# Performance work log

Measured on AMD Instinct MI355X. Metric: run time of the kernel, lower is better.

Reference implementation:

```python
import jax, jax.numpy as jnp
import numpy as np

# Dimensions (match init_kwargs / input_specs)
N, C_IN, C, H, W = 2, 256, 256, 80, 80
G, KS = 16, 3                 # groups, kernel_size
K = KS * KS                   # sampling points per group
CG = C // G                   # channels per group
PAD, STRIDE, DIL = 1, 1, 1
OFFSET_SCALE = 1.0
EPS = 1e-5                    # BatchNorm2d eps (eval mode)


def setup_inputs() -> dict:
    key = jax.random.key(0)
    ks = jax.random.split(key, 12)
    rn = lambda k, shape, s=0.02: jax.random.normal(k, shape, dtype=jnp.float32) * s
    return {
        "x": jax.random.normal(ks[0], (N, C_IN, H, W), dtype=jnp.float32),
        # Conv(inc, ouc, k=1): 1x1 conv (bias=False) + BN + SiLU
        "w1": rn(ks[1], (C_IN, C)),
        "bn1_g": jnp.ones((C,), jnp.float32), "bn1_b": jnp.zeros((C,), jnp.float32),
        "bn1_m": rn(ks[2], (C,), 0.1),
        "bn1_v": jax.random.uniform(ks[3], (C,), minval=0.5, maxval=1.5, dtype=jnp.float32),
        # DCNv4: value_proj, fused offset_mask, output_proj
        "wv": rn(ks[4], (C, C)), "bv": jnp.zeros((C,), jnp.float32),
        "wom": rn(ks[5], (C, G * K * 3)), "bom": rn(ks[6], (G * K * 3,), 0.1),
        "wo": rn(ks[7], (C, C)), "bo": jnp.zeros((C,), jnp.float32),
        # trailing BatchNorm2d + SiLU
        "bn2_g": jnp.ones((C,), jnp.float32), "bn2_b": jnp.zeros((C,), jnp.float32),
        "bn2_m": rn(ks[8], (C,), 0.1),
        "bn2_v": jax.random.uniform(ks[9], (C,), minval=0.5, maxval=1.5, dtype=jnp.float32),
    }


def _bn(x, g, b, m, v):
    # eval-mode BatchNorm over last (channel) axis
    return (x - m) * jax.lax.rsqrt(v + EPS) * g + b


def _forward(x, w1, bn1_g, bn1_b, bn1_m, bn1_v, wv, bv, wom, bom, wo, bo,
             bn2_g, bn2_b, bn2_m, bn2_v):
    # --- Conv 1x1 + BN + SiLU (channels-last) ---
    h = jnp.einsum('nchw,cd->nhwd', x, w1)                 # (N,H,W,C)
    h = jax.nn.silu(_bn(h, bn1_g, bn1_b, bn1_m, bn1_v))

    # --- DCNv4 ---
    xf = h.reshape(N, H * W, C)
    value = (xf @ wv + bv).reshape(N, H, W, G, CG)         # value projection
    om = (xf @ wom + bom).reshape(N, H, W, G, 3 * K)       # fused offset+mask
    offset = om[..., :2 * K].reshape(N, H, W, G, K, 2) * OFFSET_SCALE  # (x,y) pairs
    mask = om[..., 2 * K:]                                 # (N,H,W,G,K); v4: no softmax

    # sampling pixel coords: p = out_pos*stride - pad + kernel_offset*dil + learned offset
    ky, kx = jnp.meshgrid(jnp.arange(KS), jnp.arange(KS), indexing='ij')
    ky = (ky.reshape(-1) * DIL).astype(jnp.float32)        # (K,)
    kx = (kx.reshape(-1) * DIL).astype(jnp.float32)
    base_y = (jnp.arange(H) * STRIDE - PAD).astype(jnp.float32)
    base_x = (jnp.arange(W) * STRIDE - PAD).astype(jnp.float32)
    py = base_y[None, :, None, None, None] + ky[None, None, None, None, :] + offset[..., 1]
    px = base_x[None, None, :, None, None] + kx[None, None, None, None, :] + offset[..., 0]

    y0 = jnp.floor(py); x0 = jnp.floor(px)
    wy = py - y0;       wx = px - x0
    y0i = y0.astype(jnp.int32); x0i = x0.astype(jnp.int32)
    y1i = y0i + 1;             x1i = x0i + 1

    ni = jnp.arange(N)[:, None, None, None, None]
    gi = jnp.arange(G)[None, None, None, :, None]

    def gather(yi, xi):
        valid = ((yi >= 0) & (yi < H) & (xi >= 0) & (xi < W)).astype(value.dtype)
        v = value[ni, jnp.clip(yi, 0, H - 1), jnp.clip(xi, 0, W - 1), gi]  # (N,H,W,G,K,CG)
        return v, valid

    acc = jnp.zeros((N, H, W, G, CG), dtype=value.dtype)
    for yi, xi, wgt in ((y0i, x0i, (1 - wy) * (1 - wx)),
                        (y0i, x1i, (1 - wy) * wx),
                        (y1i, x0i, wy * (1 - wx)),
                        (y1i, x1i, wy * wx)):
        v, valid = gather(yi, xi)
        acc = acc + jnp.einsum('nhwgk,nhwgkc->nhwgc', mask * wgt * valid, v)

    out = acc.reshape(N, H * W, C) @ wo + bo               # output projection
    out = out.reshape(N, H, W, C)

    # --- BN + SiLU (wrapper tail) ---
    out = jax.nn.silu(_bn(out, bn2_g, bn2_b, bn2_m, bn2_v))
    return jnp.transpose(out, (0, 3, 1, 2))                # (N,C,H,W)


def reference(x, w1, bn1_g, bn1_b, bn1_m, bn1_v, wv, bv, wom, bom, wo, bo,
              bn2_g, bn2_b, bn2_m, bn2_v):
    return _forward(x, w1, bn1_g, bn1_b, bn1_m, bn1_v, wv, bv, wom, bom,
                    wo, bo, bn2_g, bn2_b, bn2_m, bn2_v)
```

## Files before the change

kernel.cpp:

```cpp
#include <hip/hip_runtime.h>
#include <hip/hip_bf16.h>
#include <math.h>

typedef __attribute__((ext_vector_type(8))) short bf16x8;
typedef __attribute__((ext_vector_type(4))) float f32x4;

#define NB   2
#define CC   256
#define HH   80
#define WW   80
#define HWSZ 6400
#define MM   (NB * HWSZ)
#define NCAT 768
#define EPSB 1e-5f

__global__ __launch_bounds__(256) void transpose_x_k(
    const float* __restrict__ in, __hip_bfloat16* __restrict__ outp)
{
    __shared__ float tile[32][33];
    const float* inz = in + (size_t)256 * HWSZ * blockIdx.z;
    __hip_bfloat16* outz = outp + (size_t)HWSZ * 256 * blockIdx.z;
    int bc = blockIdx.x * 32, br = blockIdx.y * 32;
    int tx = threadIdx.x & 31, ty = threadIdx.x >> 5;
#pragma unroll
    for (int i = 0; i < 32; i += 8)
        tile[ty + i][tx] = inz[(size_t)(br + ty + i) * HWSZ + bc + tx];
    __syncthreads();
#pragma unroll
    for (int i = 0; i < 32; i += 8)
        outz[(size_t)(bc + ty + i) * 256 + br + tx] =
            __float2bfloat16(tile[tx][ty + i]);
}

__device__ inline void t32g(const float* __restrict__ in, int inld, int scol0,
                            int ncols, __hip_bfloat16* __restrict__ out,
                            int orow0, int r0, int tid)
{
    __shared__ float tile[32][33];
    int tx = tid & 31, ty = tid >> 5;
#pragma unroll
    for (int i = 0; i < 32; i += 8)
        tile[ty + i][tx] = (tx < ncols)
            ? in[(size_t)(r0 + ty + i) * inld + scol0 + tx] : 0.f;
    __syncthreads();
#pragma unroll
    for (int i = 0; i < 32; i += 8)
        out[(size_t)(orow0 + ty + i) * 256 + r0 + tx] =
            __float2bfloat16(tile[tx][ty + i]);
}

__global__ __launch_bounds__(256) void prep_weights_k(
    const float* __restrict__ w1, const float* __restrict__ wv,
    const float* __restrict__ wom, const float* __restrict__ wo,
    const float* __restrict__ bv, const float* __restrict__ bom,
    __hip_bfloat16* __restrict__ w1T, __hip_bfloat16* __restrict__ BcatT,
    __hip_bfloat16* __restrict__ woT, float* __restrict__ bcat)
{
    int b = blockIdx.x, t = threadIdx.x;
    if (b < 64) {
        t32g(w1, 256, (b >> 3) * 32, 32, w1T, (b >> 3) * 32, (b & 7) * 32, t);
    } else if (b < 128) {
        int b2 = b - 64;
        t32g(wv, 256, (b2 >> 3) * 32, 32, BcatT, (b2 >> 3) * 32, (b2 & 7) * 32, t);
    } else if (b < 192) {
        int b2 = b - 128;
        t32g(wo, 256, (b2 >> 3) * 32, 32, woT, (b2 >> 3) * 32, (b2 & 7) * 32, t);
    } else if (b < 320) {
        int b2 = b - 192;
        int g = b2 >> 3, ct = b2 & 7;
        t32g(wom, 432, g * 27, 27, BcatT + 256 * 256, g * 32, ct * 32, t);
    } else {
        bcat[t] = bv[t];
#pragma unroll
        for (int j = 0; j < 2; ++j) {
            int r = j * 256 + t;
            int g = r >> 5, jj = r & 31;
            bcat[256 + r] = (jj < 27) ? bom[g * 27 + jj] : 0.f;
        }
    }
}

template <int EPI>
__global__ __launch_bounds__(256) void gemm_mfma(
    const short* __restrict__ A, const short* __restrict__ Bt,
    const float* __restrict__ bias,
    const float* __restrict__ bng, const float* __restrict__ bnb,
    const float* __restrict__ bnm, const float* __restrict__ bnv,
    void* __restrict__ Cout, int ldC)
{
    __shared__ __align__(16) char smem[49152];
    short* As = (short*)smem;
    short* Bs = (short*)(smem + 16384);

    const int t = threadIdx.x;
    const int w = t >> 6, l = t & 63;
    const int wr = w >> 1, wc = w & 1;
    const int m0 = blockIdx.x * 64, n0 = blockIdx.y * 128;

    f32x4 acc[2][4] = {};

    auto STAGE = [&](int b, int k0) {
        short* AsB = As + b * 4096;
        short* BsB = Bs + b * 8192;
#pragma unroll
        for (int i = 0; i < 2; ++i) {
            int s = (w << 1) + i;
            int c = (s << 6) + l;
            int row = c >> 3, ch = c & 7;
            const short* ga = A + (size_t)(m0 + row) * 256 + k0 + (ch << 3);
            __builtin_amdgcn_global_load_lds(
                (const __attribute__((address_space(1))) void*)ga,
                (__attribute__((address_space(3))) void*)(AsB + (s << 9)), 16, 0, 0);
        }
#pragma unroll
        for (int i = 0; i < 4; ++i) {
            int s = (w << 2) + i;
            int c = (s << 6) + l;
            int row = c >> 3, ch = c & 7;
            const short* gb = Bt + (size_t)(n0 + row) * 256 + k0 + (ch << 3);
            __builtin_amdgcn_global_load_lds(
                (const __attribute__((address_space(1))) void*)gb,
                (__attribute__((address_space(3))) void*)(BsB + (s << 9)), 16, 0, 0);
        }
    };

    auto COMPUTE = [&](int b) {
        const short* AsB = As + b * 4096;
        const short* BsB = Bs + b * 8192;
#pragma unroll
        for (int kk = 0; kk < 2; ++kk) {
            bf16x8 af[2], bfr[4];
#pragma unroll
            for (int mi = 0; mi < 2; ++mi)
                af[mi] = *(const bf16x8*)(AsB + (wr * 32 + mi * 16 + (l & 15)) * 64 +
                                          kk * 32 + ((l >> 4) << 3));
#pragma unroll
            for (int ni = 0; ni < 4; ++ni)
                bfr[ni] = *(const bf16x8*)(BsB + (wc * 64 + ni * 16 + (l & 15)) * 64 +
                                           kk * 32 + ((l >> 4) << 3));
#pragma unroll
            for (int mi = 0; mi < 2; ++mi)
#pragma unroll
                for (int ni = 0; ni < 4; ++ni)
                    acc[mi][ni] = __builtin_amdgcn_mfma_f32_16x16x32_bf16(
                        af[mi], bfr[ni], acc[mi][ni], 0, 0, 0);
        }
    };

    STAGE(0, 0);
    __syncthreads();
#pragma unroll
    for (int tt = 0; tt < 4; ++tt) {
        if (tt < 3) STAGE((tt + 1) & 1, (tt + 1) * 64);
        COMPUTE(tt & 1);
        __syncthreads();
    }

    if (EPI == 0) {
#pragma unroll
        for (int ni = 0; ni < 4; ++ni) {
            int chn = n0 + wc * 64 + ni * 16 + (l & 15);
            float bb = bias[chn];
#pragma unroll
            for (int mi = 0; mi < 2; ++mi) {
                int mbase = m0 + wr * 32 + mi * 16 + ((l >> 4) << 2);
#pragma unroll
                for (int j = 0; j < 4; ++j) {
                    float v = acc[mi][ni][j] + bb;
                    ((__hip_bfloat16*)Cout)[(size_t)(mbase + j) * ldC + chn] =
                        __float2bfloat16(v);
                }
            }
        }
    } else if (EPI == 1) {
#pragma unroll
        for (int ni = 0; ni < 4; ++ni) {
            int chn = n0 + wc * 64 + ni * 16 + (l & 15);
            float mu = bnm[chn], iv = rsqrtf(bnv[chn] + EPSB);
            float gm = bng[chn], bt = bnb[chn];
#pragma unroll
            for (int mi = 0; mi < 2; ++mi) {
                int mbase = m0 + wr * 32 + mi * 16 + ((l >> 4) << 2);
#pragma unroll
                for (int j = 0; j < 4; ++j) {
                    float v = acc[mi][ni][j];
                    v = (v - mu) * iv * gm + bt;
                    v = v / (1.f + __expf(-v));
                    ((__hip_bfloat16*)Cout)[(size_t)(mbase + j) * ldC + chn] =
                        __float2bfloat16(v);
                }
            }
        }
    } else {
        float(*CtT)[68] = (float(*)[68])smem;
        const int nimg = m0 / HWSZ;
        const int p0 = m0 % HWSZ;
#pragma unroll
        for (int h2 = 0; h2 < 2; ++h2) {
            if (wc == h2) {
#pragma unroll
                for (int ni = 0; ni < 4; ++ni)
#pragma unroll
                    for (int mi = 0; mi < 2; ++mi)
#pragma unroll
                        for (int j = 0; j < 4; ++j)
                            CtT[ni * 16 + (l & 15)]
                               [wr * 32 + mi * 16 + ((l >> 4) << 2) + j] =
                                   acc[mi][ni][j];
            }
            __syncthreads();
#pragma unroll
            for (int it = 0; it < 4; ++it) {
                int e4 = it * 256 + t;
                int row = e4 >> 4;
                int c4 = e4 & 15;
                int chn = n0 + h2 * 64 + row;
                float bb = bias[chn];
                float mu = bnm[chn], iv = rsqrtf(bnv[chn] + EPSB);
                float gm = bng[chn], bt = bnb[chn];
                f32x4 v = *(f32x4*)&CtT[row][c4 * 4];
#pragma unroll
                for (int j = 0; j < 4; ++j) {
                    float u = v[j] + bb;
                    u = (u - mu) * iv * gm + bt;
                    u = u / (1.f + __expf(-u));
                    v[j] = u;
                }
                *(f32x4*)&((float*)Cout)[(size_t)(nimg * CC + chn) * HWSZ + p0 + c4 * 4] = v;
            }
            __syncthreads();
        }
    }
}

__device__ inline void fma16(float* acc, const __hip_bfloat16* ptr, float wgt)
{
    bf16x8 v0 = *(const bf16x8*)ptr;
    bf16x8 v1 = *(const bf16x8*)(ptr + 8);
#pragma unroll
    for (int j = 0; j < 8; ++j) {
        union { unsigned u; float f; } cv;
        cv.u = ((unsigned)(unsigned short)v0[j]) << 16;
        acc[j] = fmaf(wgt, cv.f, acc[j]);
    }
#pragma unroll
    for (int j = 0; j < 8; ++j) {
        union { unsigned u; float f; } cv;
        cv.u = ((unsigned)(unsigned short)v1[j]) << 16;
        acc[8 + j] = fmaf(wgt, cv.f, acc[8 + j]);
    }
}

__global__ __launch_bounds__(256) void dcn_sample_k(
    const __hip_bfloat16* __restrict__ C2, __hip_bfloat16* __restrict__ accb)
{
    const int idx = blockIdx.x * 256 + threadIdx.x;
    const int g = idx & 15;
    const int mp = idx >> 4;
    const int p = mp % HWSZ;
    const int n = mp / HWSZ;
    const int y = p / WW, x = p % WW;

    const unsigned* omw =
        (const unsigned*)(C2 + (size_t)mp * NCAT + 256 + g * 32);
    const __hip_bfloat16* vb =
        C2 + (size_t)n * HWSZ * NCAT + g * 16;

    float mk[9];
    {
        unsigned mw[5];
#pragma unroll
        for (int i = 0; i < 5; ++i) mw[i] = omw[9 + i];
#pragma unroll
        for (int i = 0; i < 9; ++i) {
            unsigned w16 = (i & 1) ? (mw[i >> 1] >> 16) : (mw[i >> 1] & 0xffffu);
            union { unsigned u; float f; } cv; cv.u = w16 << 16;
            mk[i] = cv.f;
        }
    }

    float acc[16] = {};
#pragma unroll
    for (int k = 0; k < 9; ++k) {
        unsigned ow = omw[k];
        union { unsigned u; float f; } cx, cy;
        cx.u = (ow & 0xffffu) << 16;
        cy.u = ow & 0xffff0000u;
        float px = (float)(x - 1 + (k % 3)) + cx.f;
        float py = (float)(y - 1 + (k / 3)) + cy.f;
        float fx = floorf(px), fy = floorf(py);
        float wx = px - fx, wy = py - fy;
        int x0 = (int)fx, y0 = (int)fy;
        int x1 = x0 + 1, y1 = y0 + 1;
        float ax0 = ((unsigned)x0 < (unsigned)WW) ? (1.f - wx) : 0.f;
        float ax1 = ((unsigned)x1 < (unsigned)WW) ? wx : 0.f;
        float ay0 = ((unsigned)y0 < (unsigned)HH) ? mk[k] * (1.f - wy) : 0.f;
        float ay1 = ((unsigned)y1 < (unsigned)HH) ? mk[k] * wy : 0.f;
        int xc0 = min(max(x0, 0), WW - 1);
        int xc1 = min(max(x1, 0), WW - 1);
        int yc0 = min(max(y0, 0), HH - 1);
        int yc1 = min(max(y1, 0), HH - 1);
        const __hip_bfloat16* r0 = vb + (size_t)(yc0 * WW) * NCAT;
        const __hip_bfloat16* r1 = vb + (size_t)(yc1 * WW) * NCAT;
        fma16(acc, r0 + (size_t)xc0 * NCAT, ay0 * ax0);
        fma16(acc, r0 + (size_t)xc1 * NCAT, ay0 * ax1);
        fma16(acc, r1 + (size_t)xc0 * NCAT, ay1 * ax0);
        fma16(acc, r1 + (size_t)xc1 * NCAT, ay1 * ax1);
    }

    __hip_bfloat16* op = accb + (size_t)mp * CC + g * 16;
    bf16x8 ov0, ov1;
#pragma unroll
    for (int j = 0; j < 8; ++j) {
        __hip_bfloat16 b0 = __float2bfloat16(acc[j]);
        __hip_bfloat16 b1 = __float2bfloat16(acc[8 + j]);
        ov0[j] = *reinterpret_cast<short*>(&b0);
        ov1[j] = *reinterpret_cast<short*>(&b1);
    }
    *(bf16x8*)op = ov0;
    *(bf16x8*)(op + 8) = ov1;
}

extern "C" void kernel_launch(void* const* d_in, const int* in_sizes, int n_in,
                              void* d_out, int out_size, void* d_ws, size_t ws_size,
                              hipStream_t stream)
{
    const float* x    = (const float*)d_in[0];
    const float* w1   = (const float*)d_in[1];
    const float* bn1g = (const float*)d_in[2];
    const float* bn1b = (const float*)d_in[3];
    const float* bn1m = (const float*)d_in[4];
    const float* bn1v = (const float*)d_in[5];
    const float* wv   = (const float*)d_in[6];
    const float* bv   = (const float*)d_in[7];
    const float* wom  = (const float*)d_in[8];
    const float* bom  = (const float*)d_in[9];
    const float* wo   = (const float*)d_in[10];
    const float* bo   = (const float*)d_in[11];
    const float* bn2g = (const float*)d_in[12];
    const float* bn2b = (const float*)d_in[13];
    const float* bn2m = (const float*)d_in[14];
    const float* bn2v = (const float*)d_in[15];
    float* out = (float*)d_out;

    char* w = (char*)d_ws;
    __hip_bfloat16* xT    = (__hip_bfloat16*)(w);
    __hip_bfloat16* hbuf  = (__hip_bfloat16*)(w + 6553600);
    __hip_bfloat16* C2    = (__hip_bfloat16*)(w + 13107200);
    __hip_bfloat16* accb  = (__hip_bfloat16*)(w + 32768000);
    __hip_bfloat16* w1T   = (__hip_bfloat16*)(w + 39321600);
    __hip_bfloat16* woT   = (__hip_bfloat16*)(w + 39452672);
    __hip_bfloat16* BcatT = (__hip_bfloat16*)(w + 39583744);
    float*          bcat  = (float*)(w + 39976960);

    dim3 blk(256);

    prep_weights_k<<<dim3(321), blk, 0, stream>>>(
        w1, wv, wom, wo, bv, bom, w1T, BcatT, woT, bcat);
    transpose_x_k<<<dim3(200, 8, 2), blk, 0, stream>>>(x, xT);

    gemm_mfma<1><<<dim3(200, 2), blk, 0, stream>>>(
        (const short*)xT, (const short*)w1T, nullptr,
        bn1g, bn1b, bn1m, bn1v, hbuf, CC);
    gemm_mfma<0><<<dim3(200, 6), blk, 0, stream>>>(
        (const short*)hbuf, (const short*)BcatT, bcat,
        nullptr, nullptr, nullptr, nullptr, C2, NCAT);
    dcn_sample_k<<<dim3(MM * 16 / 256), blk, 0, stream>>>(C2, accb);
    gemm_mfma<2><<<dim3(200, 2), blk, 0, stream>>>(
        (const short*)accb, (const short*)woT, bo,
        bn2g, bn2b, bn2m, bn2v, out, 0);
}
```

Baseline: 150.6 us.

## Fuse deformable sampling into output-projection GEMM and merge prep kernels

The bilinear deformable sampling now writes its bf16 results straight into shared memory as the A tile of the output-projection GEMM, which runs in a new 512-thread kernel covering all 256 output channels per 64-row block. This removes the global round trip through the intermediate accb buffer and one kernel launch. Separately, the x transpose and the weight prep are merged into one launch. In exchange, only 200 blocks with 96KB of LDS each run for the gather-heavy stage, which may limit occupancy and latency hiding compared with the former standalone sampling kernel.

Result: no change. 148.9 us (-1.1%).

```diff
diff --git a/kernel.cpp b/kernel.cpp
--- a/kernel.cpp
+++ b/kernel.cpp
@@ -14,24 +14,6 @@
 #define NCAT 768
 #define EPSB 1e-5f
 
-__global__ __launch_bounds__(256) void transpose_x_k(
-    const float* __restrict__ in, __hip_bfloat16* __restrict__ outp)
-{
-    __shared__ float tile[32][33];
-    const float* inz = in + (size_t)256 * HWSZ * blockIdx.z;
-    __hip_bfloat16* outz = outp + (size_t)HWSZ * 256 * blockIdx.z;
-    int bc = blockIdx.x * 32, br = blockIdx.y * 32;
-    int tx = threadIdx.x & 31, ty = threadIdx.x >> 5;
-#pragma unroll
-    for (int i = 0; i < 32; i += 8)
-        tile[ty + i][tx] = inz[(size_t)(br + ty + i) * HWSZ + bc + tx];
-    __syncthreads();
-#pragma unroll
-    for (int i = 0; i < 32; i += 8)
-        outz[(size_t)(bc + ty + i) * 256 + br + tx] =
-            __float2bfloat16(tile[tx][ty + i]);
-}
-
 __device__ inline void t32g(const float* __restrict__ in, int inld, int scol0,
                             int ncols, __hip_bfloat16* __restrict__ out,
                             int orow0, int r0, int tid)
@@ -49,14 +31,35 @@
             __float2bfloat16(tile[tx][ty + i]);
 }
 
-__global__ __launch_bounds__(256) void prep_weights_k(
+__global__ __launch_bounds__(256) void prep_all_k(
+    const float* __restrict__ x,
     const float* __restrict__ w1, const float* __restrict__ wv,
     const float* __restrict__ wom, const float* __restrict__ wo,
     const float* __restrict__ bv, const float* __restrict__ bom,
+    __hip_bfloat16* __restrict__ xT,
     __hip_bfloat16* __restrict__ w1T, __hip_bfloat16* __restrict__ BcatT,
     __hip_bfloat16* __restrict__ woT, float* __restrict__ bcat)
 {
     int b = blockIdx.x, t = threadIdx.x;
+    if (b < 3200) {
+        __shared__ float tile[32][33];
+        int z = b / 1600, r = b % 1600;
+        int by = r / 200, bx = r % 200;
+        const float* inz = x + (size_t)256 * HWSZ * z;
+        __hip_bfloat16* outz = xT + (size_t)HWSZ * 256 * z;
+        int bc = bx * 32, br = by * 32;
+        int tx = t & 31, ty = t >> 5;
+#pragma unroll
+        for (int i = 0; i < 32; i += 8)
+            tile[ty + i][tx] = inz[(size_t)(br + ty + i) * HWSZ + bc + tx];
+        __syncthreads();
+#pragma unroll
+        for (int i = 0; i < 32; i += 8)
+            outz[(size_t)(bc + ty + i) * 256 + br + tx] =
+                __float2bfloat16(tile[tx][ty + i]);
+        return;
+    }
+    b -= 3200;
     if (b < 64) {
         t32g(w1, 256, (b >> 3) * 32, 32, w1T, (b >> 3) * 32, (b & 7) * 32, t);
     } else if (b < 128) {
@@ -172,7 +175,7 @@
                 }
             }
         }
-    } else if (EPI == 1) {
+    } else {
 #pragma unroll
         for (int ni = 0; ni < 4; ++ni) {
             int chn = n0 + wc * 64 + ni * 16 + (l & 15);
@@ -191,134 +194,190 @@
                 }
             }
         }
-    } else {
-        float(*CtT)[68] = (float(*)[68])smem;
-        const int nimg = m0 / HWSZ;
-        const int p0 = m0 % HWSZ;
-#pragma unroll
-        for (int h2 = 0; h2 < 2; ++h2) {
-            if (wc == h2) {
+    }
+}
+
+__global__ __launch_bounds__(512) void gemm3_fused_k(
+    const __hip_bfloat16* __restrict__ C2, const short* __restrict__ woT,
+    const float* __restrict__ bias,
+    const float* __restrict__ bng, const float* __restrict__ bnb,
+    const float* __restrict__ bnm, const float* __restrict__ bnv,
+    float* __restrict__ out)
+{
+    __shared__ __align__(16) char smem[98304];
+    short* As = (short*)smem;
+    short* Bs = (short*)(smem + 32768);
+
+    const int t = threadIdx.x;
+    const int w = t >> 6, l = t & 63;
+    const int wr = w >> 2, wc = w & 3;
+    const int m0 = blockIdx.x * 64;
+    const int nimg = m0 / HWSZ;
+    const int p0 = m0 % HWSZ;
+
+    auto STAGE_B = [&](int b, int k0) {
+        short* BsB = Bs + b * 16384;
+#pragma unroll
+        for (int i = 0; i < 4; ++i) {
+            int c = t + i * 512;
+            int row = c >> 3, ch = c & 7;
+            const short* gb = woT + (size_t)row * 256 + k0 + (ch << 3);
+            __builtin_amdgcn_global_load_lds(
+                (const __attribute__((address_space(1))) void*)gb,
+                (__attribute__((address_space(3))) void*)(BsB + ((w << 6) + (i << 9)) * 8),
+                16, 0, 0);
+        }
+    };
+
+    STAGE_B(0, 0);
+
+#pragma unroll
+    for (int it = 0; it < 2; ++it) {
+        int task = it * 512 + t;
+        int g = task & 15, px = task >> 4;
+        int mp = m0 + px;
+        int p = mp % HWSZ;
+        int y = p / WW, x = p % WW;
+
+        const unsigned* omw =
+            (const unsigned*)(C2 + (size_t)mp * NCAT + 256 + g * 32);
+        const __hip_bfloat16* vb = C2 + (size_t)nimg * HWSZ * NCAT + g * 16;
+
+        float mk[9];
+        {
+            unsigned mw[5];
+#pragma unroll
+            for (int i = 0; i < 5; ++i) mw[i] = omw[9 + i];
+#pragma unroll
+            for (int i = 0; i < 9; ++i) {
+                unsigned w16 = (i & 1) ? (mw[i >> 1] >> 16) : (mw[i >> 1] & 0xffffu);
+                union { unsigned u; float f; } cv; cv.u = w16 << 16;
+                mk[i] = cv.f;
+            }
+        }
+
+        float acc[16] = {};
+#pragma unroll
+        for (int k = 0; k < 9; ++k) {
+            unsigned ow = omw[k];
+            union { unsigned u; float f; } cx, cy;
+            cx.u = (ow & 0xffffu) << 16;
+            cy.u = ow & 0xffff0000u;
+            float px_ = (float)(x - 1 + (k % 3)) + cx.f;
+            float py_ = (float)(y - 1 + (k / 3)) + cy.f;
+            float fx = floorf(px_), fy = floorf(py_);
+            float wx = px_ - fx, wy = py_ - fy;
+            int x0 = (int)fx, y0 = (int)fy;
+            int x1 = x0 + 1, y1 = y0 + 1;
+            float ax0 = ((unsigned)x0 < (unsigned)WW) ? (1.f - wx) : 0.f;
+            float ax1 = ((unsigned)x1 < (unsigned)WW) ? wx : 0.f;
+            float ay0 = ((unsigned)y0 < (unsigned)HH) ? mk[k] * (1.f - wy) : 0.f;
+            float ay1 = ((unsigned)y1 < (unsigned)HH) ? mk[k] * wy : 0.f;
+            int xc0 = min(max(x0, 0), WW - 1);
+            int xc1 = min(max(x1, 0), WW - 1);
+            int yc0 = min(max(y0, 0), HH - 1);
+            int yc1 = min(max(y1, 0), HH - 1);
+            const __hip_bfloat16* r0 = vb + (size_t)(yc0 * WW) * NCAT;
+            const __hip_bfloat16* r1 = vb + (size_t)(yc1 * WW) * NCAT;
+            const __hip_bfloat16* pts[4] = {
+                r0 + (size_t)xc0 * NCAT, r0 + (size_t)xc1 * NCAT,
+                r1 + (size_t)xc0 * NCAT, r1 + (size_t)xc1 * NCAT };
+            float wgt[4] = { ay0 * ax0, ay0 * ax1, ay1 * ax0, ay1 * ax1 };
+#pragma unroll
+            for (int q = 0; q < 4; ++q) {
+                bf16x8 v0 = *(const bf16x8*)pts[q];
+                bf16x8 v1 = *(const bf16x8*)(pts[q] + 8);
+#pragma unroll
+                for (int j = 0; j < 8; ++j) {
+                    union { unsigned u; float f; } cv;
+                    cv.u = ((unsigned)(unsigned short)v0[j]) << 16;
+                    acc[j] = fmaf(wgt[q], cv.f, acc[j]);
+                }
+#pragma unroll
+                for (int j = 0; j < 8; ++j) {
+                    union { unsigned u; float f; } cv;
+                    cv.u = ((unsigned)(unsigned short)v1[j]) << 16;
+                    acc[8 + j] = fmaf(wgt[q], cv.f, acc[8 + j]);
+                }
+            }
+        }
+
+        bf16x8 ov0, ov1;
+#pragma unroll
+        for (int j = 0; j < 8; ++j) {
+            __hip_bfloat16 b0 = __float2bfloat16(acc[j]);
+            __hip_bfloat16 b1 = __float2bfloat16(acc[8 + j]);
+            ov0[j] = *reinterpret_cast<short*>(&b0);
+            ov1[j] = *reinterpret_cast<short*>(&b1);
+        }
+        *(bf16x8*)(As + px * 256 + g * 16) = ov0;
+        *(bf16x8*)(As + px * 256 + g * 16 + 8) = ov1;
+    }
+    __syncthreads();
+
+    f32x4 acc[2][4] = {};
+#pragma unroll
+    for (int tt = 0; tt < 4; ++tt) {
+        if (tt < 3) STAGE_B((tt + 1) & 1, (tt + 1) * 64);
+        const short* BsB = Bs + (tt & 1) * 16384;
+        const int k0 = tt * 64;
+#pragma unroll
+        for (int kk = 0; kk < 2; ++kk) {
+            bf16x8 af[2], bfr[4];
+#pragma unroll
+            for (int mi = 0; mi < 2; ++mi)
+                af[mi] = *(const bf16x8*)(As + (wr * 32 + mi * 16 + (l & 15)) * 256 +
+                                          k0 + kk * 32 + ((l >> 4) << 3));
+#pragma unroll
+            for (int ni = 0; ni < 4; ++ni)
+                bfr[ni] = *(const bf16x8*)(BsB + (wc * 64 + ni * 16 + (l & 15)) * 64 +
+                                           kk * 32 + ((l >> 4) << 3));
+#pragma unroll
+            for (int mi = 0; mi < 2; ++mi)
 #pragma unroll
                 for (int ni = 0; ni < 4; ++ni)
-#pragma unroll
-                    for (int mi = 0; mi < 2; ++mi)
-#pragma unroll
-                        for (int j = 0; j < 4; ++j)
-                            CtT[ni * 16 + (l & 15)]
-                               [wr * 32 + mi * 16 + ((l >> 4) << 2) + j] =
-                                   acc[mi][ni][j];
+                    acc[mi][ni] = __builtin_amdgcn_mfma_f32_16x16x32_bf16(
+                        af[mi], bfr[ni], acc[mi][ni], 0, 0, 0);
+        }
+        __syncthreads();
+    }
+
+    float(*CtT)[68] = (float(*)[68])smem;
+#pragma unroll
+    for (int h2 = 0; h2 < 4; ++h2) {
+        if (wc == h2) {
+#pragma unroll
+            for (int ni = 0; ni < 4; ++ni)
+#pragma unroll
+                for (int mi = 0; mi < 2; ++mi)
+#pragma unroll
+                    for (int j = 0; j < 4; ++j)
+                        CtT[ni * 16 + (l & 15)]
+                           [wr * 32 + mi * 16 + ((l >> 4) << 2) + j] =
+                               acc[mi][ni][j];
+        }
+        __syncthreads();
+#pragma unroll
+        for (int it = 0; it < 2; ++it) {
+            int e4 = it * 512 + t;
+            int row = e4 >> 4;
+            int c4 = e4 & 15;
+            int chn = h2 * 64 + row;
+            float bb = bias[chn];
+            float mu = bnm[chn], iv = rsqrtf(bnv[chn] + EPSB);
+            float gm = bng[chn], bt = bnb[chn];
+            f32x4 v = *(f32x4*)&CtT[row][c4 * 4];
+#pragma unroll
+            for (int j = 0; j < 4; ++j) {
+                float u = v[j] + bb;
+                u = (u - mu) * iv * gm + bt;
+                u = u / (1.f + __expf(-u));
+                v[j] = u;
             }
-            __syncthreads();
-#pragma unroll
-            for (int it = 0; it < 4; ++it) {
-                int e4 = it * 256 + t;
-                int row = e4 >> 4;
-                int c4 = e4 & 15;
-                int chn = n0 + h2 * 64 + row;
-                float bb = bias[chn];
-                float mu = bnm[chn], iv = rsqrtf(bnv[chn] + EPSB);
-                float gm = bng[chn], bt = bnb[chn];
-                f32x4 v = *(f32x4*)&CtT[row][c4 * 4];
-#pragma unroll
-                for (int j = 0; j < 4; ++j) {
-                    float u = v[j] + bb;
-                    u = (u - mu) * iv * gm + bt;
-                    u = u / (1.f + __expf(-u));
-                    v[j] = u;
-                }
-                *(f32x4*)&((float*)Cout)[(size_t)(nimg * CC + chn) * HWSZ + p0 + c4 * 4] = v;
-            }
-            __syncthreads();
-        }
-    }
-}
-
-__device__ inline void fma16(float* acc, const __hip_bfloat16* ptr, float wgt)
-{
-    bf16x8 v0 = *(const bf16x8*)ptr;
-    bf16x8 v1 = *(const bf16x8*)(ptr + 8);
-#pragma unroll
-    for (int j = 0; j < 8; ++j) {
-        union { unsigned u; float f; } cv;
-        cv.u = ((unsigned)(unsigned short)v0[j]) << 16;
-        acc[j] = fmaf(wgt, cv.f, acc[j]);
-    }
-#pragma unroll
-    for (int j = 0; j < 8; ++j) {
-        union { unsigned u; float f; } cv;
-        cv.u = ((unsigned)(unsigned short)v1[j]) << 16;
-        acc[8 + j] = fmaf(wgt, cv.f, acc[8 + j]);
-    }
-}
-
-__global__ __launch_bounds__(256) void dcn_sample_k(
-    const __hip_bfloat16* __restrict__ C2, __hip_bfloat16* __restrict__ accb)
-{
-    const int idx = blockIdx.x * 256 + threadIdx.x;
-    const int g = idx & 15;
-    const int mp = idx >> 4;
-    const int p = mp % HWSZ;
-    const int n = mp / HWSZ;
-    const int y = p / WW, x = p % WW;
-
-    const unsigned* omw =
-        (const unsigned*)(C2 + (size_t)mp * NCAT + 256 + g * 32);
-    const __hip_bfloat16* vb =
-        C2 + (size_t)n * HWSZ * NCAT + g * 16;
-
-    float mk[9];
-    {
-        unsigned mw[5];
-#pragma unroll
-        for (int i = 0; i < 5; ++i) mw[i] = omw[9 + i];
-#pragma unroll
-        for (int i = 0; i < 9; ++i) {
-            unsigned w16 = (i & 1) ? (mw[i >> 1] >> 16) : (mw[i >> 1] & 0xffffu);
-            union { unsigned u; float f; } cv; cv.u = w16 << 16;
-            mk[i] = cv.f;
-        }
-    }
-
-    float acc[16] = {};
-#pragma unroll
-    for (int k = 0; k < 9; ++k) {
-        unsigned ow = omw[k];
-        union { unsigned u; float f; } cx, cy;
-        cx.u = (ow & 0xffffu) << 16;
-        cy.u = ow & 0xffff0000u;
-        float px = (float)(x - 1 + (k % 3)) + cx.f;
-        float py = (float)(y - 1 + (k / 3)) + cy.f;
-        float fx = floorf(px), fy = floorf(py);
-        float wx = px - fx, wy = py - fy;
-        int x0 = (int)fx, y0 = (int)fy;
-        int x1 = x0 + 1, y1 = y0 + 1;
-        float ax0 = ((unsigned)x0 < (unsigned)WW) ? (1.f - wx) : 0.f;
-        float ax1 = ((unsigned)x1 < (unsigned)WW) ? wx : 0.f;
-        float ay0 = ((unsigned)y0 < (unsigned)HH) ? mk[k] * (1.f - wy) : 0.f;
-        float ay1 = ((unsigned)y1 < (unsigned)HH) ? mk[k] * wy : 0.f;
-        int xc0 = min(max(x0, 0), WW - 1);
-        int xc1 = min(max(x1, 0), WW - 1);
-        int yc0 = min(max(y0, 0), HH - 1);
-        int yc1 = min(max(y1, 0), HH - 1);
-        const __hip_bfloat16* r0 = vb + (size_t)(yc0 * WW) * NCAT;
-        const __hip_bfloat16* r1 = vb + (size_t)(yc1 * WW) * NCAT;
-        fma16(acc, r0 + (size_t)xc0 * NCAT, ay0 * ax0);
-        fma16(acc, r0 + (size_t)xc1 * NCAT, ay0 * ax1);
-        fma16(acc, r1 + (size_t)xc0 * NCAT, ay1 * ax0);
-        fma16(acc, r1 + (size_t)xc1 * NCAT, ay1 * ax1);
-    }
-
-    __hip_bfloat16* op = accb + (size_t)mp * CC + g * 16;
-    bf16x8 ov0, ov1;
-#pragma unroll
-    for (int j = 0; j < 8; ++j) {
-        __hip_bfloat16 b0 = __float2bfloat16(acc[j]);
-        __hip_bfloat16 b1 = __float2bfloat16(acc[8 + j]);
-        ov0[j] = *reinterpret_cast<short*>(&b0);
-        ov1[j] = *reinterpret_cast<short*>(&b1);
-    }
-    *(bf16x8*)op = ov0;
-    *(bf16x8*)(op + 8) = ov1;
+            *(f32x4*)&out[(size_t)(nimg * CC + chn) * HWSZ + p0 + c4 * 4] = v;
+        }
+        __syncthreads();
+    }
 }
 
 extern "C" void kernel_launch(void* const* d_in, const int* in_sizes, int n_in,
@@ -347,7 +406,6 @@
     __hip_bfloat16* xT    = (__hip_bfloat16*)(w);
     __hip_bfloat16* hbuf  = (__hip_bfloat16*)(w + 6553600);
     __hip_bfloat16* C2    = (__hip_bfloat16*)(w + 13107200);
-    __hip_bfloat16* accb  = (__hip_bfloat16*)(w + 32768000);
     __hip_bfloat16* w1T   = (__hip_bfloat16*)(w + 39321600);
     __hip_bfloat16* woT   = (__hip_bfloat16*)(w + 39452672);
     __hip_bfloat16* BcatT = (__hip_bfloat16*)(w + 39583744);
@@ -355,18 +413,17 @@
 
     dim3 blk(256);
 
-    prep_weights_k<<<dim3(321), blk, 0, stream>>>(
-        w1, wv, wom, wo, bv, bom, w1T, BcatT, woT, bcat);
-    transpose_x_k<<<dim3(200, 8, 2), blk, 0, stream>>>(x, xT);
+    prep_all_k<<<dim3(3521), blk, 0, stream>>>(
+        x, w1, wv, wom, wo, bv, bom, xT, w1T, BcatT, woT, bcat);
 
     gemm_mfma<1><<<dim3(200, 2), blk, 0, stream>>>(
         (const short*)xT, (const short*)w1T, nullptr,
         bn1g, bn1b, bn1m, bn1v, hbuf, CC);
+
     gemm_mfma<0><<<dim3(200, 6), blk, 0, stream>>>(
         (const short*)hbuf, (const short*)BcatT, bcat,
         nullptr, nullptr, nullptr, nullptr, C2, NCAT);
-    dcn_sample_k<<<dim3(MM * 16 / 256), blk, 0, stream>>>(C2, accb);
-    gemm_mfma<2><<<dim3(200, 2), blk, 0, stream>>>(
-        (const short*)accb, (const short*)woT, bo,
-        bn2g, bn2b, bn2m, bn2v, out, 0);
+
+    gemm3_fused_k<<<dim3(200), dim3(512), 0, stream>>>(
+        C2, (const short*)woT, bo, bn2g, bn2b, bn2m, bn2v, out);
 }
```

## Shrink GEMM tiles to 32x128 with K=32 stages and fuse x transpose into prep

Applied to the files above, without the earlier changes.

The GEMM kernel now uses 32-row M tiles with each of four waves covering 32 columns, and steps K in chunks of 32 over 8 double-buffered stages instead of 64 over 4. This cuts LDS to 20KB and doubles the grid for more blocks and occupancy. The cost is less reuse per tile and twice as many barriers. The x transpose kernel is merged into the weight prep kernel to save one launch.

Result: no change. 150.4 us (-0.1%).

```diff
diff --git a/kernel.cpp b/kernel.cpp
--- a/kernel.cpp
+++ b/kernel.cpp
@@ -14,24 +14,6 @@
 #define NCAT 768
 #define EPSB 1e-5f
 
-__global__ __launch_bounds__(256) void transpose_x_k(
-    const float* __restrict__ in, __hip_bfloat16* __restrict__ outp)
-{
-    __shared__ float tile[32][33];
-    const float* inz = in + (size_t)256 * HWSZ * blockIdx.z;
-    __hip_bfloat16* outz = outp + (size_t)HWSZ * 256 * blockIdx.z;
-    int bc = blockIdx.x * 32, br = blockIdx.y * 32;
-    int tx = threadIdx.x & 31, ty = threadIdx.x >> 5;
-#pragma unroll
-    for (int i = 0; i < 32; i += 8)
-        tile[ty + i][tx] = inz[(size_t)(br + ty + i) * HWSZ + bc + tx];
-    __syncthreads();
-#pragma unroll
-    for (int i = 0; i < 32; i += 8)
-        outz[(size_t)(bc + ty + i) * 256 + br + tx] =
-            __float2bfloat16(tile[tx][ty + i]);
-}
-
 __device__ inline void t32g(const float* __restrict__ in, int inld, int scol0,
                             int ncols, __hip_bfloat16* __restrict__ out,
                             int orow0, int r0, int tid)
@@ -49,14 +31,35 @@
             __float2bfloat16(tile[tx][ty + i]);
 }
 
-__global__ __launch_bounds__(256) void prep_weights_k(
+__global__ __launch_bounds__(256) void prep_all_k(
+    const float* __restrict__ x,
     const float* __restrict__ w1, const float* __restrict__ wv,
     const float* __restrict__ wom, const float* __restrict__ wo,
     const float* __restrict__ bv, const float* __restrict__ bom,
+    __hip_bfloat16* __restrict__ xT,
     __hip_bfloat16* __restrict__ w1T, __hip_bfloat16* __restrict__ BcatT,
     __hip_bfloat16* __restrict__ woT, float* __restrict__ bcat)
 {
     int b = blockIdx.x, t = threadIdx.x;
+    if (b < 3200) {
+        __shared__ float tile[32][33];
+        int z = b / 1600, r = b % 1600;
+        int by = r / 200, bx = r % 200;
+        const float* inz = x + (size_t)256 * HWSZ * z;
+        __hip_bfloat16* outz = xT + (size_t)HWSZ * 256 * z;
+        int bc = bx * 32, br = by * 32;
+        int tx = t & 31, ty = t >> 5;
+#pragma unroll
+        for (int i = 0; i < 32; i += 8)
+            tile[ty + i][tx] = inz[(size_t)(br + ty + i) * HWSZ + bc + tx];
+        __syncthreads();
+#pragma unroll
+        for (int i = 0; i < 32; i += 8)
+            outz[(size_t)(bc + ty + i) * 256 + br + tx] =
+                __float2bfloat16(tile[tx][ty + i]);
+        return;
+    }
+    b -= 3200;
     if (b < 64) {
         t32g(w1, 256, (b >> 3) * 32, 32, w1T, (b >> 3) * 32, (b & 7) * 32, t);
     } else if (b < 128) {
@@ -88,147 +91,119 @@
     const float* __restrict__ bnm, const float* __restrict__ bnv,
     void* __restrict__ Cout, int ldC)
 {
-    __shared__ __align__(16) char smem[49152];
+    __shared__ __align__(16) char smem[20480];
     short* As = (short*)smem;
-    short* Bs = (short*)(smem + 16384);
+    short* Bs = (short*)(smem + 4096);
 
     const int t = threadIdx.x;
     const int w = t >> 6, l = t & 63;
-    const int wr = w >> 1, wc = w & 1;
-    const int m0 = blockIdx.x * 64, n0 = blockIdx.y * 128;
-
-    f32x4 acc[2][4] = {};
+    const int wc = w;
+    const int m0 = blockIdx.x * 32, n0 = blockIdx.y * 128;
+
+    f32x4 acc[2][2] = {};
 
     auto STAGE = [&](int b, int k0) {
-        short* AsB = As + b * 4096;
-        short* BsB = Bs + b * 8192;
-#pragma unroll
-        for (int i = 0; i < 2; ++i) {
-            int s = (w << 1) + i;
-            int c = (s << 6) + l;
-            int row = c >> 3, ch = c & 7;
+        short* AsB = As + b * 1024;
+        short* BsB = Bs + b * 4096;
+        if (t < 128) {
+            int row = t >> 2, ch = t & 3;
             const short* ga = A + (size_t)(m0 + row) * 256 + k0 + (ch << 3);
             __builtin_amdgcn_global_load_lds(
                 (const __attribute__((address_space(1))) void*)ga,
-                (__attribute__((address_space(3))) void*)(AsB + (s << 9)), 16, 0, 0);
-        }
-#pragma unroll
-        for (int i = 0; i < 4; ++i) {
-            int s = (w << 2) + i;
-            int c = (s << 6) + l;
-            int row = c >> 3, ch = c & 7;
+                (__attribute__((address_space(3))) void*)(AsB + t * 8), 16, 0, 0);
+        }
+#pragma unroll
+        for (int i = 0; i < 2; ++i) {
+            int c = t + i * 256;
+            int row = c >> 2, ch = c & 3;
             const short* gb = Bt + (size_t)(n0 + row) * 256 + k0 + (ch << 3);
             __builtin_amdgcn_global_load_lds(
                 (const __attribute__((address_space(1))) void*)gb,
-                (__attribute__((address_space(3))) void*)(BsB + (s << 9)), 16, 0, 0);
-        }
-    };
-
-    auto COMPUTE = [&](int b) {
-        const short* AsB = As + b * 4096;
-        const short* BsB = Bs + b * 8192;
-#pragma unroll
-        for (int kk = 0; kk < 2; ++kk) {
-            bf16x8 af[2], bfr[4];
-#pragma unroll
-            for (int mi = 0; mi < 2; ++mi)
-                af[mi] = *(const bf16x8*)(AsB + (wr * 32 + mi * 16 + (l & 15)) * 64 +
-                                          kk * 32 + ((l >> 4) << 3));
-#pragma unroll
-            for (int ni = 0; ni < 4; ++ni)
-                bfr[ni] = *(const bf16x8*)(BsB + (wc * 64 + ni * 16 + (l & 15)) * 64 +
-                                           kk * 32 + ((l >> 4) << 3));
-#pragma unroll
-            for (int mi = 0; mi < 2; ++mi)
-#pragma unroll
-                for (int ni = 0; ni < 4; ++ni)
-                    acc[mi][ni] = __builtin_amdgcn_mfma_f32_16x16x32_bf16(
-                        af[mi], bfr[ni], acc[mi][ni], 0, 0, 0);
+                (__attribute__((address_space(3))) void*)(BsB + c * 8), 16, 0, 0);
         }
     };
 
     STAGE(0, 0);
     __syncthreads();
 #pragma unroll
-    for (int tt = 0; tt < 4; ++tt) {
-        if (tt < 3) STAGE((tt + 1) & 1, (tt + 1) * 64);
-        COMPUTE(tt & 1);
+    for (int tt = 0; tt < 8; ++tt) {
+        if (tt < 7) STAGE((tt + 1) & 1, (tt + 1) * 32);
+        const short* AsB = As + (tt & 1) * 1024;
+        const short* BsB = Bs + (tt & 1) * 4096;
+        bf16x8 af[2], bfr[2];
+#pragma unroll
+        for (int mi = 0; mi < 2; ++mi)
+            af[mi] = *(const bf16x8*)(AsB + (mi * 16 + (l & 15)) * 32 +
+                                      ((l >> 4) << 3));
+#pragma unroll
+        for (int ni = 0; ni < 2; ++ni)
+            bfr[ni] = *(const bf16x8*)(BsB + (wc * 32 + ni * 16 + (l & 15)) * 32 +
+                                       ((l >> 4) << 3));
+#pragma unroll
+        for (int mi = 0; mi < 2; ++mi)
+#pragma unroll
+            for (int ni = 0; ni < 2; ++ni)
+                acc[mi][ni] = __builtin_amdgcn_mfma_f32_16x16x32_bf16(
+                    af[mi], bfr[ni], acc[mi][ni], 0, 0, 0);
         __syncthreads();
     }
 
-    if (EPI == 0) {
-#pragma unroll
-        for (int ni = 0; ni < 4; ++ni) {
-            int chn = n0 + wc * 64 + ni * 16 + (l & 15);
-            float bb = bias[chn];
+    if (EPI == 0 || EPI == 1) {
+#pragma unroll
+        for (int ni = 0; ni < 2; ++ni) {
+            int chn = n0 + wc * 32 + ni * 16 + (l & 15);
+            float bb = (EPI == 0) ? bias[chn] : 0.f;
+            float mu = 0.f, iv = 0.f, gm = 0.f, bt2 = 0.f;
+            if (EPI == 1) {
+                mu = bnm[chn]; iv = rsqrtf(bnv[chn] + EPSB);
+                gm = bng[chn]; bt2 = bnb[chn];
+            }
 #pragma unroll
             for (int mi = 0; mi < 2; ++mi) {
-                int mbase = m0 + wr * 32 + mi * 16 + ((l >> 4) << 2);
+                int mbase = m0 + mi * 16 + ((l >> 4) << 2);
 #pragma unroll
                 for (int j = 0; j < 4; ++j) {
                     float v = acc[mi][ni][j] + bb;
+                    if (EPI == 1) {
+                        v = (v - mu) * iv * gm + bt2;
+                        v = v / (1.f + __expf(-v));
+                    }
                     ((__hip_bfloat16*)Cout)[(size_t)(mbase + j) * ldC + chn] =
                         __float2bfloat16(v);
                 }
             }
         }
-    } else if (EPI == 1) {
-#pragma unroll
-        for (int ni = 0; ni < 4; ++ni) {
-            int chn = n0 + wc * 64 + ni * 16 + (l & 15);
-            float mu = bnm[chn], iv = rsqrtf(bnv[chn] + EPSB);
-            float gm = bng[chn], bt = bnb[chn];
-#pragma unroll
-            for (int mi = 0; mi < 2; ++mi) {
-                int mbase = m0 + wr * 32 + mi * 16 + ((l >> 4) << 2);
-#pragma unroll
-                for (int j = 0; j < 4; ++j) {
-                    float v = acc[mi][ni][j];
-                    v = (v - mu) * iv * gm + bt;
-                    v = v / (1.f + __expf(-v));
-                    ((__hip_bfloat16*)Cout)[(size_t)(mbase + j) * ldC + chn] =
-                        __float2bfloat16(v);
-                }
-            }
-        }
     } else {
-        float(*CtT)[68] = (float(*)[68])smem;
+        float(*CtT)[36] = (float(*)[36])smem;
         const int nimg = m0 / HWSZ;
         const int p0 = m0 % HWSZ;
 #pragma unroll
-        for (int h2 = 0; h2 < 2; ++h2) {
-            if (wc == h2) {
-#pragma unroll
-                for (int ni = 0; ni < 4; ++ni)
-#pragma unroll
-                    for (int mi = 0; mi < 2; ++mi)
-#pragma unroll
-                        for (int j = 0; j < 4; ++j)
-                            CtT[ni * 16 + (l & 15)]
-                               [wr * 32 + mi * 16 + ((l >> 4) << 2) + j] =
-                                   acc[mi][ni][j];
+        for (int ni = 0; ni < 2; ++ni)
+#pragma unroll
+            for (int mi = 0; mi < 2; ++mi)
+#pragma unroll
+                for (int j = 0; j < 4; ++j)
+                    CtT[wc * 32 + ni * 16 + (l & 15)]
+                       [mi * 16 + ((l >> 4) << 2) + j] = acc[mi][ni][j];
+        __syncthreads();
+#pragma unroll
+        for (int it = 0; it < 4; ++it) {
+            int e4 = it * 256 + t;
+            int row = e4 >> 3;
+            int c4 = e4 & 7;
+            int chn = n0 + row;
+            float bb = bias[chn];
+            float mu = bnm[chn], iv = rsqrtf(bnv[chn] + EPSB);
+            float gm = bng[chn], bt2 = bnb[chn];
+            f32x4 v = *(f32x4*)&CtT[row][c4 * 4];
+#pragma unroll
+            for (int j = 0; j < 4; ++j) {
+                float u = v[j] + bb;
+                u = (u - mu) * iv * gm + bt2;
+                u = u / (1.f + __expf(-u));
+                v[j] = u;
             }
-            __syncthreads();
-#pragma unroll
-            for (int it = 0; it < 4; ++it) {
-                int e4 = it * 256 + t;
-                int row = e4 >> 4;
-                int c4 = e4 & 15;
-                int chn = n0 + h2 * 64 + row;
-                float bb = bias[chn];
-                float mu = bnm[chn], iv = rsqrtf(bnv[chn] + EPSB);
-                float gm = bng[chn], bt = bnb[chn];
-                f32x4 v = *(f32x4*)&CtT[row][c4 * 4];
-#pragma unroll
-                for (int j = 0; j < 4; ++j) {
-                    float u = v[j] + bb;
-                    u = (u - mu) * iv * gm + bt;
-                    u = u / (1.f + __expf(-u));
-                    v[j] = u;
-                }
-                *(f32x4*)&((float*)Cout)[(size_t)(nimg * CC + chn) * HWSZ + p0 + c4 * 4] = v;
-            }
-            __syncthreads();
+            *(f32x4*)&((float*)Cout)[(size_t)(nimg * CC + chn) * HWSZ + p0 + c4 * 4] = v;
         }
     }
 }
@@ -355,18 +330,20 @@
 
     dim3 blk(256);
 
-    prep_weights_k<<<dim3(321), blk, 0, stream>>>(
-        w1, wv, wom, wo, bv, bom, w1T, BcatT, woT, bcat);
-    transpose_x_k<<<dim3(200, 8, 2), blk, 0, stream>>>(x, xT);
-
-    gemm_mfma<1><<<dim3(200, 2), blk, 0, stream>>>(
+    prep_all_k<<<dim3(3521), blk, 0, stream>>>(
+        x, w1, wv, wom, wo, bv, bom, xT, w1T, BcatT, woT, bcat);
+
+    gemm_mfma<1><<<dim3(400, 2), blk, 0, stream>>>(
         (const short*)xT, (const short*)w1T, nullptr,
         bn1g, bn1b, bn1m, bn1v, hbuf, CC);
-    gemm_mfma<0><<<dim3(200, 6), blk, 0, stream>>>(
+
+    gemm_mfma<0><<<dim3(400, 6), blk, 0, stream>>>(
         (const short*)hbuf, (const short*)BcatT, bcat,
         nullptr, nullptr, nullptr, nullptr, C2, NCAT);
+
     dcn_sample_k<<<dim3(MM * 16 / 256), blk, 0, stream>>>(C2, accb);
-    gemm_mfma<2><<<dim3(200, 2), blk, 0, stream>>>(
+
+    gemm_mfma<2><<<dim3(400, 2), blk, 0, stream>>>(
         (const short*)accb, (const short*)woT, bo,
         bn2g, bn2b, bn2m, bn2v, out, 0);
 }
```
